# Kernel tuning notes

Hardware: AMD Instinct MI355X
Metric: run time of the kernel (lower is better)

## Reference

```python
import jax, jax.numpy as jnp
import numpy as np

H = 16
BN_EPS = 1e-12

def setup_inputs() -> dict:
    key = jax.random.key(0)
    ks = jax.random.split(key, 12)
    B, S, D = 2, 2048, 1024
    sc_in = 1.0 / np.sqrt(D)
    inp = {
        "hidden_states": jax.random.normal(ks[0], (B, S, D), jnp.float32),
        "attention_mask": jnp.zeros((B, 1, 1, S), jnp.float32),
        "Wq": jax.random.normal(ks[1], (D, D), jnp.float32) * sc_in,
        "bq": jnp.zeros((D,), jnp.float32),
        "Wk": jax.random.normal(ks[2], (D, D), jnp.float32) * sc_in,
        "bk": jnp.zeros((D,), jnp.float32),
        "Wv": jax.random.normal(ks[3], (D, D), jnp.float32) * sc_in,
        "bv": jnp.zeros((D,), jnp.float32),
        "pW1": jax.random.normal(ks[4], (D, 64), jnp.float32) * sc_in,
        "pb1": jnp.zeros((64,), jnp.float32),
        "bn_gamma": jnp.ones((64,), jnp.float32),
        "bn_beta": jnp.zeros((64,), jnp.float32),
        "bn_mean": jnp.zeros((64,), jnp.float32),
        "bn_var": jnp.ones((64,), jnp.float32),
        "pW2": jax.random.normal(ks[5], (64, H), jnp.float32) * (1.0 / 8.0),
        "pb2": jnp.zeros((H,), jnp.float32),
    }
    return inp


def reference(hidden_states, attention_mask, Wq, bq, Wk, bk, Wv, bv,
              pW1, pb1, bn_gamma, bn_beta, bn_mean, bn_var, pW2, pb2):
    B, S, D = hidden_states.shape
    hd = D // H
    scale = 1.0 / jnp.sqrt(jnp.asarray(hd, hidden_states.dtype))

    def split_heads(x):  # [B,S,D] -> [B,H,S,hd]
        return x.reshape(B, S, H, hd).transpose(0, 2, 1, 3)

    q = split_heads(hidden_states @ Wq + bq)
    k = split_heads(hidden_states @ Wk + bk)
    v = split_heads(hidden_states @ Wv + bv)

    scores = jnp.einsum("bhqd,bhkd->bhqk", q, k) * scale + attention_mask
    probs = jax.nn.softmax(scores, axis=-1)

    # head-gate predictor (layer_id == 0 -> mean pooling over sequence)
    pooled = jnp.mean(hidden_states, axis=1)  # [B,D]
    h = pooled @ pW1 + pb1
    h = (h - bn_mean) * jax.lax.rsqrt(bn_var + BN_EPS) * bn_gamma + bn_beta
    h = jax.nn.relu(h)
    logits = h @ pW2 + pb2  # [B,H]
    # inference-mode gumbel gate: hard threshold at 0
    head_gate = (logits >= 0).astype(probs.dtype)  # [B,H]

    probs = probs * head_gate[:, :, None, None]
    ctx = jnp.einsum("bhqk,bhkd->bhqd", probs, v)
    return ctx.transpose(0, 2, 1, 3).reshape(B, S, D)
```

## Files before the change

### kernel.cpp

```cpp
#include <hip/hip_runtime.h>

#define S_LEN 2048
#define D_DIM 1024
#define NH 16
#define HD 64
#define BATCH 2

#define QK_SCALE 0.18033688011112042f
#define LOG2E 1.4426950408889634f

using s16x8 = __attribute__((ext_vector_type(8))) short;
using u16x8 = __attribute__((ext_vector_type(8))) unsigned short;
using f32x4 = __attribute__((ext_vector_type(4))) float;
using bf16x8v = __attribute__((ext_vector_type(8))) __bf16;

typedef const __attribute__((address_space(1))) unsigned int* gas_ptr;
typedef __attribute__((address_space(3))) unsigned int* las_ptr;

__device__ __forceinline__ unsigned short f32_to_bf16(float f) {
  unsigned int u = __float_as_uint(f);
  u += 0x7FFFu + ((u >> 16) & 1u);
  return (unsigned short)(u >> 16);
}

__device__ __forceinline__ f32x4 mfma_bf16(s16x8 a, s16x8 b, f32x4 c) {
  return __builtin_amdgcn_mfma_f32_16x16x32_bf16(
      __builtin_bit_cast(bf16x8v, a), __builtin_bit_cast(bf16x8v, b), c, 0, 0, 0);
}

__device__ __forceinline__ float exp2_fast(float x) {
  float r;
  asm("v_exp_f32 %0, %1" : "=v"(r) : "v"(x));
  return r;
}

__device__ __forceinline__ unsigned int cvt_pk_bf16(float a, float b) {
  unsigned int r;
  asm("v_cvt_pk_bf16_f32 %0, %1, %2" : "=v"(r) : "v"(a), "v"(b));
  return r;
}

__global__ __launch_bounds__(256) void pool_cvt(const float* __restrict__ hs,
                                                unsigned short* __restrict__ hsb,
                                                float* __restrict__ partial) {
  int bid = blockIdx.x;
  int b = bid & 1;
  int chunk = (bid >> 1) & 7;
  int dq = bid >> 4;
  int d = dq * 256 + threadIdx.x;
  const float* p = hs + ((size_t)b * S_LEN + chunk * 256) * D_DIM + d;
  unsigned short* o = hsb + ((size_t)b * S_LEN + chunk * 256) * D_DIM + d;
  float s = 0.f;
  for (int i = 0; i < 256; ++i) {
    float v = p[(size_t)i * D_DIM];
    s += v;
    o[(size_t)i * D_DIM] = f32_to_bf16(v);
  }
  partial[(b * 8 + chunk) * D_DIM + d] = s;
}

__global__ __launch_bounds__(256) void transpose_w3(
    const float* __restrict__ Wq, const float* __restrict__ Wk,
    const float* __restrict__ Wv, unsigned short* __restrict__ WTq,
    unsigned short* __restrict__ WTk, unsigned short* __restrict__ WTv) {
  __shared__ float tile[32][33];
  int z = blockIdx.z;
  const float* W = (z == 0) ? Wq : (z == 1) ? Wk : Wv;
  unsigned short* WT = (z == 0) ? WTq : (z == 1) ? WTk : WTv;
  float scale = (z == 0) ? QK_SCALE : 1.0f;
  int tx = threadIdx.x & 31;
  int ty = threadIdx.x >> 5;
  int c0 = blockIdx.x * 32;
  int r0 = blockIdx.y * 32;
#pragma unroll
  for (int i = 0; i < 4; ++i)
    tile[ty + i * 8][tx] = W[(r0 + ty + i * 8) * D_DIM + c0 + tx];
  __syncthreads();
#pragma unroll
  for (int i = 0; i < 4; ++i)
    WT[(c0 + ty + i * 8) * D_DIM + r0 + tx] = f32_to_bf16(tile[tx][ty + i * 8] * scale);
}

__global__ __launch_bounds__(512) void gate_kernel(
    const float* __restrict__ partial, const float* __restrict__ pW1,
    const float* __restrict__ pb1, const float* __restrict__ gamma,
    const float* __restrict__ beta, const float* __restrict__ mean,
    const float* __restrict__ var, const float* __restrict__ pW2,
    const float* __restrict__ pb2, float* __restrict__ gate) {
  __shared__ float pooled[2 * D_DIM];
  __shared__ float hsh[2][64];
  int t = threadIdx.x;
  for (int idx = t; idx < 2 * D_DIM; idx += 512) {
    int b = idx >> 10, k = idx & 1023;
    float s = 0.f;
#pragma unroll
    for (int c = 0; c < 8; ++c) s += partial[(b * 8 + c) * D_DIM + k];
    pooled[idx] = s * (1.0f / 2048.0f);
  }
  __syncthreads();
  int b = t >> 8, jj = (t >> 2) & 63, quarter = t & 3;
  float acc = 0.f;
  for (int k = quarter * 256; k < quarter * 256 + 256; ++k)
    acc += pooled[b * D_DIM + k] * pW1[k * 64 + jj];
  acc += __shfl_xor(acc, 1, 64);
  acc += __shfl_xor(acc, 2, 64);
  if (quarter == 0) {
    acc += pb1[jj];
    acc = (acc - mean[jj]) * rsqrtf(var[jj] + 1e-12f) * gamma[jj] + beta[jj];
    hsh[b][jj] = fmaxf(acc, 0.f);
  }
  __syncthreads();
  if (t < 32) {
    int bb = t >> 4, hh = t & 15;
    float lg = pb2[hh];
#pragma unroll
    for (int kk = 0; kk < 64; ++kk) lg += hsh[bb][kk] * pW2[kk * NH + hh];
    gate[bb * NH + hh] = (lg >= 0.f) ? 1.f : 0.f;
  }
}

__global__ __launch_bounds__(256) void proj_gemm3(
    const unsigned short* __restrict__ A, const unsigned short* __restrict__ BT,
    const float* __restrict__ bq, const float* __restrict__ bk,
    const float* __restrict__ bv, unsigned short* __restrict__ Qb,
    unsigned short* __restrict__ Kb, unsigned short* __restrict__ Vtb) {
  __shared__ __align__(16) unsigned short As[2][128 * 32];
  __shared__ __align__(16) unsigned short Bs[2][128 * 32];
  int idx = blockIdx.x;
  int xcd = idx & 7, j = idx >> 3;
  int xm = xcd * 4 + j / 24;
  int yn = j % 24;
  int m0 = xm * 128, n0 = yn * 128;
  int tid = threadIdx.x, wave = tid >> 6, lane = tid & 63;
  int l15 = lane & 15, lhi = lane >> 4;
  int wm = (wave >> 1) * 64, wn = (wave & 1) * 64;
  int srow = tid >> 2;
  int scol = (tid & 3) * 8;
  f32x4 acc[4][4] = {};

#define PSTAGE(BUFI, K0)                                                           \
  {                                                                                \
    _Pragma("unroll") for (int jj = 0; jj < 2; ++jj) {                             \
      __builtin_amdgcn_global_load_lds(                                            \
          (gas_ptr)(A + (size_t)(m0 + jj * 64 + srow) * D_DIM + (K0) + scol),      \
          (las_ptr)((char*)As + (BUFI) * 8192 + jj * 4096 + wave * 1024), 16, 0,   \
          0);                                                                      \
      __builtin_amdgcn_global_load_lds(                                            \
          (gas_ptr)(BT + (size_t)(n0 + jj * 64 + srow) * D_DIM + (K0) + scol),     \
          (las_ptr)((char*)Bs + (BUFI) * 8192 + jj * 4096 + wave * 1024), 16, 0,   \
          0);                                                                      \
    }                                                                              \
  }

  PSTAGE(0, 0);
  __syncthreads();

  for (int k0 = 0; k0 < D_DIM; k0 += 32) {
    int buf = (k0 >> 5) & 1;
    PSTAGE(buf ^ 1, (k0 + 32) & (D_DIM - 1));
    const char* ab = (const char*)As + buf * 8192;
    const char* bb = (const char*)Bs + buf * 8192;
    s16x8 af[4], bf[4];
#pragma unroll
    for (int mi = 0; mi < 4; ++mi)
      af[mi] = *(const s16x8*)(ab + (wm + mi * 16 + l15) * 64 + lhi * 16);
#pragma unroll
    for (int ni = 0; ni < 4; ++ni)
      bf[ni] = *(const s16x8*)(bb + (wn + ni * 16 + l15) * 64 + lhi * 16);
    __builtin_amdgcn_s_setprio(1);
#pragma unroll
    for (int mi = 0; mi < 4; ++mi)
#pragma unroll
      for (int ni = 0; ni < 4; ++ni)
        acc[mi][ni] = mfma_bf16(af[mi], bf[ni], acc[mi][ni]);
    __builtin_amdgcn_s_setprio(0);
    __syncthreads();
  }
#undef PSTAGE

#pragma unroll
  for (int mi = 0; mi < 4; ++mi)
#pragma unroll
    for (int ni = 0; ni < 4; ++ni) {
      int row0 = m0 + wm + mi * 16 + lhi * 4;
      int col = n0 + wn + ni * 16 + l15;
      int seg = col >> 10, c = col & 1023;
      if (seg == 2) {
        float bvv = bv[c];
        int h = c >> 6, d = c & 63;
        int b = row0 >> 11, s = row0 & 2047;
        ushort4 pk;
        pk.x = f32_to_bf16(acc[mi][ni][0] + bvv);
        pk.y = f32_to_bf16(acc[mi][ni][1] + bvv);
        pk.z = f32_to_bf16(acc[mi][ni][2] + bvv);
        pk.w = f32_to_bf16(acc[mi][ni][3] + bvv);
        *(ushort4*)&Vtb[((size_t)(b * NH + h) * HD + d) * S_LEN + s] = pk;
      } else {
        float bb2 = (seg == 0) ? bq[c] * QK_SCALE : bk[c];
        unsigned short* dst = (seg == 0) ? Qb : Kb;
        int h = c >> 6, d = c & 63;
#pragma unroll
        for (int r = 0; r < 4; ++r) {
          int row = row0 + r;
          int b = row >> 11, s = row & 2047;
          dst[((size_t)(b * NH + h) * S_LEN + s) * HD + d] =
              f32_to_bf16(acc[mi][ni][r] + bb2);
        }
      }
    }
}

__global__ __launch_bounds__(256) void attn_kernel(
    const unsigned short* __restrict__ Q, const unsigned short* __restrict__ K,
    const unsigned short* __restrict__ Vt, const float* __restrict__ mask,
    const float* __restrict__ gate, float* __restrict__ Out) {
  __shared__ __align__(16) unsigned short Ks[2][4096];
  __shared__ __align__(16) unsigned short Vs[2][4096];
  __shared__ __align__(16) unsigned short p_lds[4][1024];

  int idx = blockIdx.x;
  int xcd = idx & 7;
  int slot = idx >> 3;
  int qc = slot & 31;
  int r = (slot >> 5) * 8 + xcd;
  int tid = threadIdx.x;
  int wave = tid >> 6, lane = tid & 63;
  int l15 = lane & 15, lhi = lane >> 4;

  float gv = (lane < 32) ? gate[lane] : 0.f;
  unsigned long long live = __ballot(gv != 0.f);
  int W = __popcll(live);
  bool working = (r < W);
  int want = working ? r : (r - W);
  unsigned long long M = working ? live : (~live & 0xFFFFFFFFull);
  int head = 0, c = 0;
#pragma unroll
  for (int hh = 0; hh < 32; ++hh) {
    if ((M >> hh) & 1) {
      if (c == want) head = hh;
      ++c;
    }
  }
  int b = head >> 4, h = head & 15;
  int q0 = qc * 64 + wave * 16;
  int qrow = q0 + l15;

  if (!working) {
    float4 z = {0.f, 0.f, 0.f, 0.f};
    int row = qc * 64 + (tid >> 2);
    float* op = Out + ((size_t)b * S_LEN + row) * D_DIM + h * HD + (tid & 3) * 16;
#pragma unroll
    for (int dd = 0; dd < 4; ++dd) *(float4*)(op + dd * 4) = z;
    return;
  }

  const unsigned short* Qp = Q + (size_t)head * S_LEN * HD;
  const unsigned short* Kp = K + (size_t)head * S_LEN * HD;
  const unsigned short* Vp = Vt + (size_t)head * HD * S_LEN;
  const float* maskp = mask + (size_t)b * S_LEN;

  int psw = (l15 & 7) << 4;
  int oo0 = wave * 2048 + lane * 16;
  int oo1 = oo0 + 1024;
  int row0 = oo0 >> 7, row1 = oo1 >> 7;
  int e0 = ((oo0 & 127) ^ ((row0 & 7) << 4)) >> 1;
  int e1 = ((oo1 & 127) ^ ((row1 & 7) << 4)) >> 1;
  const unsigned short* kb0 = Kp + row0 * HD + e0;
  const unsigned short* kb1 = Kp + row1 * HD + e1;
  const unsigned short* vb0 = Vp + (size_t)row0 * S_LEN + e0;
  const unsigned short* vb1 = Vp + (size_t)row1 * S_LEN + e1;
  unsigned short* ksb = &Ks[0][0];
  unsigned short* vsb = &Vs[0][0];
  int w0 = (wave * 2048) >> 1;
  int w1 = w0 + 512;

#define STAGE(BUFI, KTV)                                                            \
  {                                                                                 \
    __builtin_amdgcn_global_load_lds((gas_ptr)(kb0 + (size_t)(KTV) * HD),           \
                                     (las_ptr)(ksb + (BUFI) * 4096 + w0), 16, 0, 0);\
    __builtin_amdgcn_global_load_lds((gas_ptr)(kb1 + (size_t)(KTV) * HD),           \
                                     (las_ptr)(ksb + (BUFI) * 4096 + w1), 16, 0, 0);\
    __builtin_amdgcn_global_load_lds((gas_ptr)(vb0 + (KTV)),                        \
                                     (las_ptr)(vsb + (BUFI) * 4096 + w0), 16, 0, 0);\
    __builtin_amdgcn_global_load_lds((gas_ptr)(vb1 + (KTV)),                        \
                                     (las_ptr)(vsb + (BUFI) * 4096 + w1), 16, 0, 0);\
  }

  STAGE(0, 0);
  float4 mvc[4];
#pragma unroll
  for (int nf = 0; nf < 4; ++nf)
    mvc[nf] = *(const float4*)(maskp + nf * 16 + lhi * 4);

  s16x8 q_frag[2];
#pragma unroll
  for (int ks = 0; ks < 2; ++ks)
    q_frag[ks] = *(const s16x8*)(Qp + (size_t)qrow * HD + ks * 32 + lhi * 8);

  int swz0 = (lhi * 16) ^ psw;
  int swz1 = (64 + lhi * 16) ^ psw;
  char* pbase = (char*)p_lds + wave * 2048 + l15 * 128;

  f32x4 o_acc[4] = {};
  float s_run = 0.f;

  __syncthreads();

  for (int kt = 0; kt < S_LEN; kt += 64) {
    int buf = (kt >> 6) & 1;
    int ktn = (kt + 64) & (S_LEN - 1);
    STAGE(buf ^ 1, ktn);
    float4 mvn[4];
#pragma unroll
    for (int nf = 0; nf < 4; ++nf)
      mvn[nf] = *(const float4*)(maskp + ktn + nf * 16 + lhi * 4);

    const char* kc = (const char*)ksb + buf * 8192;
    f32x4 sc[4] = {};
    __builtin_amdgcn_s_setprio(1);
#pragma unroll
    for (int nf = 0; nf < 4; ++nf) {
      int rb = (nf * 16 + l15) * 128;
      s16x8 a0 = *(const s16x8*)(kc + (rb + swz0));
      s16x8 a1 = *(const s16x8*)(kc + (rb + swz1));
      sc[nf] = mfma_bf16(a0, q_frag[0], sc[nf]);
      sc[nf] = mfma_bf16(a1, q_frag[1], sc[nf]);
    }
    __builtin_amdgcn_s_setprio(0);

    float psnf[4];
#pragma unroll
    for (int nf = 0; nf < 4; ++nf) {
#pragma unroll
      for (int rr = 0; rr < 4; ++rr)
        sc[nf][rr] = exp2_fast(fmaf(((const float*)&mvc[nf])[rr], LOG2E, sc[nf][rr]));
      psnf[nf] = (sc[nf][0] + sc[nf][1]) + (sc[nf][2] + sc[nf][3]);
    }
    s_run += (psnf[0] + psnf[1]) + (psnf[2] + psnf[3]);

#pragma unroll
    for (int nf = 0; nf < 4; ++nf) {
      uint2 pk;
      pk.x = cvt_pk_bf16(sc[nf][0], sc[nf][1]);
      pk.y = cvt_pk_bf16(sc[nf][2], sc[nf][3]);
      *(uint2*)(pbase + ((nf * 32 + lhi * 8) ^ psw)) = pk;
    }

    const char* vc = (const char*)vsb + buf * 8192;
    __builtin_amdgcn_s_setprio(1);
#pragma unroll
    for (int ks = 0; ks < 2; ++ks) {
      int sw = ks ? swz1 : swz0;
      s16x8 pf = *(const s16x8*)(pbase + ((ks * 64 + lhi * 16) ^ psw));
#pragma unroll
      for (int df = 0; df < 4; ++df) {
        s16x8 vf = *(const s16x8*)(vc + ((df * 16 + l15) * 128 + sw));
        o_acc[df] = mfma_bf16(vf, pf, o_acc[df]);
      }
    }
    __builtin_amdgcn_s_setprio(0);

    __syncthreads();
#pragma unroll
    for (int nf = 0; nf < 4; ++nf) mvc[nf] = mvn[nf];
  }
#undef STAGE

  float s_tot = s_run;
  s_tot += __shfl_xor(s_tot, 16, 64);
  s_tot += __shfl_xor(s_tot, 32, 64);
  float inv = 1.0f / s_tot;

#pragma unroll
  for (int df = 0; df < 4; ++df) {
    float4 ov;
    ov.x = o_acc[df][0] * inv;
    ov.y = o_acc[df][1] * inv;
    ov.z = o_acc[df][2] * inv;
    ov.w = o_acc[df][3] * inv;
    *(float4*)(Out + ((size_t)b * S_LEN + qrow) * D_DIM + h * HD + df * 16 + lhi * 4) = ov;
  }
}


extern "C" void kernel_launch(void* const* d_in, const int* in_sizes, int n_in,
                              void* d_out, int out_size, void* d_ws, size_t ws_size,
                              hipStream_t stream) {
  (void)in_sizes; (void)n_in; (void)out_size; (void)ws_size;
  const float* hs   = (const float*)d_in[0];
  const float* mask = (const float*)d_in[1];
  const float* Wq   = (const float*)d_in[2];
  const float* bq   = (const float*)d_in[3];
  const float* Wk   = (const float*)d_in[4];
  const float* bk   = (const float*)d_in[5];
  const float* Wv   = (const float*)d_in[6];
  const float* bv   = (const float*)d_in[7];
  const float* pW1  = (const float*)d_in[8];
  const float* pb1  = (const float*)d_in[9];
  const float* gam  = (const float*)d_in[10];
  const float* bet  = (const float*)d_in[11];
  const float* mea  = (const float*)d_in[12];
  const float* var  = (const float*)d_in[13];
  const float* pW2  = (const float*)d_in[14];
  const float* pb2  = (const float*)d_in[15];
  float* out = (float*)d_out;

  const size_t MB = 1u << 20;
  char* ws = (char*)d_ws;
  unsigned short* hsb = (unsigned short*)(ws);
  unsigned short* wTq = (unsigned short*)(ws + 8 * MB);
  unsigned short* wTk = (unsigned short*)(ws + 10 * MB);
  unsigned short* wTv = (unsigned short*)(ws + 12 * MB);
  unsigned short* Qb  = (unsigned short*)(ws + 14 * MB);
  unsigned short* Kb  = (unsigned short*)(ws + 22 * MB);
  unsigned short* Vtb = (unsigned short*)(ws + 30 * MB);
  float* partial = (float*)(ws + 38 * MB);
  float* gateb   = (float*)(ws + 38 * MB + 65536);

  pool_cvt<<<64, 256, 0, stream>>>(hs, hsb, partial);
  transpose_w3<<<dim3(32, 32, 3), 256, 0, stream>>>(Wq, Wk, Wv, wTq, wTk, wTv);
  gate_kernel<<<1, 512, 0, stream>>>(partial, pW1, pb1, gam, bet, mea, var, pW2, pb2, gateb);

  proj_gemm3<<<768, 256, 0, stream>>>(hsb, wTq, bq, bk, bv, Qb, Kb, Vtb);

  attn_kernel<<<1024, 256, 0, stream>>>(Qb, Kb, Vtb, mask, gateb, out);
}
```

Before: 153.8 us.

## Widen pool_cvt grid and use single-buffered K=64 swizzled LDS tiles in projection GEMM

pool_cvt now launches 256 blocks of 64 rows each instead of 64 blocks of 256 rows, raising parallelism for the fp32-to-bf16 conversion and pooling pass. The gate kernel reduces 32 partial sums instead of 8. The projection GEMM drops the double-buffered K=32 staging in favour of a single K=64 LDS tile with an XOR row swizzle, which reduces bank conflicts and halves the number of barrier iterations. The cost is that global loads no longer overlap with the MFMA work of the previous tile.

```diff
diff --git a/kernel.cpp b/kernel.cpp
--- a/kernel.cpp
+++ b/kernel.cpp
@@ -45,18 +45,18 @@
                                                 float* __restrict__ partial) {
   int bid = blockIdx.x;
   int b = bid & 1;
-  int chunk = (bid >> 1) & 7;
-  int dq = bid >> 4;
+  int chunk = (bid >> 1) & 31;
+  int dq = bid >> 6;
   int d = dq * 256 + threadIdx.x;
-  const float* p = hs + ((size_t)b * S_LEN + chunk * 256) * D_DIM + d;
-  unsigned short* o = hsb + ((size_t)b * S_LEN + chunk * 256) * D_DIM + d;
+  const float* p = hs + ((size_t)b * S_LEN + chunk * 64) * D_DIM + d;
+  unsigned short* o = hsb + ((size_t)b * S_LEN + chunk * 64) * D_DIM + d;
   float s = 0.f;
-  for (int i = 0; i < 256; ++i) {
+  for (int i = 0; i < 64; ++i) {
     float v = p[(size_t)i * D_DIM];
     s += v;
     o[(size_t)i * D_DIM] = f32_to_bf16(v);
   }
-  partial[(b * 8 + chunk) * D_DIM + d] = s;
+  partial[(size_t)(b * 32 + chunk) * D_DIM + d] = s;
 }
 
 __global__ __launch_bounds__(256) void transpose_w3(
@@ -94,7 +94,7 @@
     int b = idx >> 10, k = idx & 1023;
     float s = 0.f;
 #pragma unroll
-    for (int c = 0; c < 8; ++c) s += partial[(b * 8 + c) * D_DIM + k];
+    for (int c = 0; c < 32; ++c) s += partial[(size_t)(b * 32 + c) * D_DIM + k];
     pooled[idx] = s * (1.0f / 2048.0f);
   }
   __syncthreads();
@@ -124,8 +124,8 @@
     const float* __restrict__ bq, const float* __restrict__ bk,
     const float* __restrict__ bv, unsigned short* __restrict__ Qb,
     unsigned short* __restrict__ Kb, unsigned short* __restrict__ Vtb) {
-  __shared__ __align__(16) unsigned short As[2][128 * 32];
-  __shared__ __align__(16) unsigned short Bs[2][128 * 32];
+  __shared__ __align__(16) unsigned short As[128 * 64];
+  __shared__ __align__(16) unsigned short Bs[128 * 64];
   int idx = blockIdx.x;
   int xcd = idx & 7, j = idx >> 3;
   int xm = xcd * 4 + j / 24;
@@ -134,49 +134,52 @@
   int tid = threadIdx.x, wave = tid >> 6, lane = tid & 63;
   int l15 = lane & 15, lhi = lane >> 4;
   int wm = (wave >> 1) * 64, wn = (wave & 1) * 64;
-  int srow = tid >> 2;
-  int scol = (tid & 3) * 8;
   f32x4 acc[4][4] = {};
 
-#define PSTAGE(BUFI, K0)                                                           \
-  {                                                                                \
-    _Pragma("unroll") for (int jj = 0; jj < 2; ++jj) {                             \
-      __builtin_amdgcn_global_load_lds(                                            \
-          (gas_ptr)(A + (size_t)(m0 + jj * 64 + srow) * D_DIM + (K0) + scol),      \
-          (las_ptr)((char*)As + (BUFI) * 8192 + jj * 4096 + wave * 1024), 16, 0,   \
-          0);                                                                      \
-      __builtin_amdgcn_global_load_lds(                                            \
-          (gas_ptr)(BT + (size_t)(n0 + jj * 64 + srow) * D_DIM + (K0) + scol),     \
-          (las_ptr)((char*)Bs + (BUFI) * 8192 + jj * 4096 + wave * 1024), 16, 0,   \
-          0);                                                                      \
-    }                                                                              \
-  }
-
-  PSTAGE(0, 0);
-  __syncthreads();
-
-  for (int k0 = 0; k0 < D_DIM; k0 += 32) {
-    int buf = (k0 >> 5) & 1;
-    PSTAGE(buf ^ 1, (k0 + 32) & (D_DIM - 1));
-    const char* ab = (const char*)As + buf * 8192;
-    const char* bb = (const char*)Bs + buf * 8192;
-    s16x8 af[4], bf[4];
-#pragma unroll
-    for (int mi = 0; mi < 4; ++mi)
-      af[mi] = *(const s16x8*)(ab + (wm + mi * 16 + l15) * 64 + lhi * 16);
-#pragma unroll
-    for (int ni = 0; ni < 4; ++ni)
-      bf[ni] = *(const s16x8*)(bb + (wn + ni * 16 + l15) * 64 + lhi * 16);
+  const unsigned short* asrc[4];
+  const unsigned short* bsrc[4];
+  int ldst[4];
+#pragma unroll
+  for (int r4 = 0; r4 < 4; ++r4) {
+    int o = tid * 16 + r4 * 4096;
+    int row = o >> 7;
+    int e = ((o & 127) ^ ((row & 7) << 4)) >> 1;
+    asrc[r4] = A + (size_t)(m0 + row) * D_DIM + e;
+    bsrc[r4] = BT + (size_t)(n0 + row) * D_DIM + e;
+    ldst[r4] = o >> 1;
+  }
+  int rsw = (l15 & 7) << 4;
+
+  for (int k0 = 0; k0 < D_DIM; k0 += 64) {
+#pragma unroll
+    for (int r4 = 0; r4 < 4; ++r4) {
+      __builtin_amdgcn_global_load_lds((gas_ptr)(asrc[r4] + k0),
+                                       (las_ptr)(As + ldst[r4]), 16, 0, 0);
+      __builtin_amdgcn_global_load_lds((gas_ptr)(bsrc[r4] + k0),
+                                       (las_ptr)(Bs + ldst[r4]), 16, 0, 0);
+    }
+    __syncthreads();
     __builtin_amdgcn_s_setprio(1);
 #pragma unroll
-    for (int mi = 0; mi < 4; ++mi)
+    for (int ks = 0; ks < 2; ++ks) {
+      s16x8 af[4], bf[4];
+#pragma unroll
+      for (int mi = 0; mi < 4; ++mi)
+        af[mi] = *(const s16x8*)((const char*)As + (wm + mi * 16 + l15) * 128 +
+                                 ((ks * 64 + lhi * 16) ^ rsw));
 #pragma unroll
       for (int ni = 0; ni < 4; ++ni)
-        acc[mi][ni] = mfma_bf16(af[mi], bf[ni], acc[mi][ni]);
+        bf[ni] = *(const s16x8*)((const char*)Bs + (wn + ni * 16 + l15) * 128 +
+                                 ((ks * 64 + lhi * 16) ^ rsw));
+#pragma unroll
+      for (int mi = 0; mi < 4; ++mi)
+#pragma unroll
+        for (int ni = 0; ni < 4; ++ni)
+          acc[mi][ni] = mfma_bf16(af[mi], bf[ni], acc[mi][ni]);
+    }
     __builtin_amdgcn_s_setprio(0);
     __syncthreads();
   }
-#undef PSTAGE
 
 #pragma unroll
   for (int mi = 0; mi < 4; ++mi)
@@ -415,9 +418,9 @@
   unsigned short* Kb  = (unsigned short*)(ws + 22 * MB);
   unsigned short* Vtb = (unsigned short*)(ws + 30 * MB);
   float* partial = (float*)(ws + 38 * MB);
-  float* gateb   = (float*)(ws + 38 * MB + 65536);
-
-  pool_cvt<<<64, 256, 0, stream>>>(hs, hsb, partial);
+  float* gateb   = (float*)(ws + 38 * MB + 262144);
+
+  pool_cvt<<<256, 256, 0, stream>>>(hs, hsb, partial);
   transpose_w3<<<dim3(32, 32, 3), 256, 0, stream>>>(Wq, Wk, Wv, wTq, wTk, wTv);
   gate_kernel<<<1, 512, 0, stream>>>(partial, pW1, pb1, gam, bet, mea, var, pW2, pb2, gateb);
 
```

Result: faster. 130.1 us (-15.4%).
